# Optimization experiments

Measured on AMD Instinct MI355X. Metric: run time of the kernel, lower is better.

## Reference

```python
import jax, jax.numpy as jnp
import numpy as np

N_NODES = 50000
N_EDGES = 600000
D = 128  # input_nf = output_nf = hidden_nf
EDGE_IN = 2 * D + 1   # source, target, radial
NODE_IN = 2 * D       # x, agg


def _glorot(key, shape):
    fan_in, fan_out = shape[0], shape[1]
    lim = float(np.sqrt(6.0 / (fan_in + fan_out)))
    return jax.random.uniform(key, shape, jnp.float32, -lim, lim)


def setup_inputs() -> dict:
    key = jax.random.key(0)
    ks = jax.random.split(key, 16)
    h = jax.random.normal(ks[0], (N_NODES, D), jnp.float32)
    edge_index = jax.random.randint(ks[1], (2, N_EDGES), 0, N_NODES, jnp.int64 if jax.config.read('jax_enable_x64') else jnp.int32)
    coord = jax.random.uniform(ks[2], (N_NODES, 3), jnp.float32)
    l = jnp.array([10.0, 10.0, 10.0], jnp.float32)  # periodic box lengths (non-trainable buffer)
    return {
        'h': h, 'edge_index': edge_index, 'coord': coord, 'num_nodes': N_NODES, 'l': l,
        # edge_mlp: Linear(257,128) SiLU Linear(128,128) SiLU
        'We1': _glorot(ks[3], (EDGE_IN, D)), 'be1': jnp.zeros((D,), jnp.float32),
        'We2': _glorot(ks[4], (D, D)),       'be2': jnp.zeros((D,), jnp.float32),
        # node_mlp: Linear(256,128) SiLU Linear(128,128)
        'Wn1': _glorot(ks[5], (NODE_IN, D)), 'bn1': jnp.zeros((D,), jnp.float32),
        'Wn2': _glorot(ks[6], (D, D)),       'bn2': jnp.zeros((D,), jnp.float32),
        # coord_mlp: Linear(128,128) SiLU Linear(128,1, bias=False, xavier gain=0.001)
        'Wc1': _glorot(ks[7], (D, D)),       'bc1': jnp.zeros((D,), jnp.float32),
        'Wc2': _glorot(ks[8], (D, 1)) * 0.001,
    }


def reference(h, edge_index, coord, num_nodes, l,
              We1, be1, We2, be2, Wn1, bn1, Wn2, bn2, Wc1, bc1, Wc2):
    row, col = edge_index[0], edge_index[1]

    # coord2radial with periodic minimum-image wrap
    diff = coord[row] - coord[col]                       # [E, 3]
    diff = jnp.where(diff > 0.5 * l, diff - l, diff)
    diff = jnp.where(diff < -0.5 * l, diff + l, diff)
    radial = jnp.sum(diff * diff, axis=1, keepdims=True)  # [E, 1]

    # edge model: gather -> concat -> 2-layer SiLU MLP
    eh = jnp.concatenate([h[row], h[col], radial], axis=1)  # [E, 257]
    eh = jax.nn.silu(eh @ We1 + be1)
    edge_feat = jax.nn.silu(eh @ We2 + be2)                 # [E, 128]

    # coord model: trans/agg computed in the original but discarded (dead code);
    # only the periodic remainder of coord is returned.
    coord_out = jnp.remainder(coord, l)

    # node model: scatter-add edge features into nodes, then MLP + residual
    agg = jax.ops.segment_sum(edge_feat, row, num_segments=num_nodes)  # [N, 128]
    nh = jnp.concatenate([h, agg], axis=1)                              # [N, 256]
    nh = jax.nn.silu(nh @ Wn1 + bn1)
    h_out = h + (nh @ Wn2 + bn2)

    return h_out, coord_out, edge_feat
```

## Files before the change

kernel.cpp:

```cpp
#include <hip/hip_runtime.h>
#include <math.h>

#define D 128
#define SXS 264
#define SHS 132
#define SFS 132

typedef unsigned int u32;
typedef unsigned short u16;
typedef __attribute__((ext_vector_type(8))) short bf16x8;
typedef __attribute__((ext_vector_type(4))) float f32x4;

__device__ __forceinline__ float bfl(u32 u) { return __uint_as_float(u << 16); }
__device__ __forceinline__ float bfh(u32 u) { return __uint_as_float(u & 0xFFFF0000u); }
__device__ __forceinline__ u16 f2bf(float f) {
    u32 u = __float_as_uint(f);
    return (u16)((u + 0x7FFFu + ((u >> 16) & 1u)) >> 16);
}
__device__ __forceinline__ u32 cvt_pk_bf16(float lo, float hi) {
    u32 r;
    asm("v_cvt_pk_bf16_f32 %0, %1, %2" : "=v"(r) : "v"(lo), "v"(hi));
    return r;
}
__device__ __forceinline__ u16 cvt1_bf16(float v) { return (u16)cvt_pk_bf16(v, v); }
__device__ __forceinline__ float silu_f(float x) { return x / (1.0f + __expf(-x)); }

__global__ void coord_kernel(const float* __restrict__ coord,
                             const float* __restrict__ lbox,
                             float* __restrict__ out, int n3) {
    int i = blockIdx.x * 256 + threadIdx.x;
    if (i < n3) {
        float ld = lbox[i % 3];
        float c = coord[i];
        float r = fmodf(c, ld);
        if (r < 0.f) r += ld;
        out[i] = r;
    }
}

__global__ void prep_weights(const float* __restrict__ We1, const float* __restrict__ We2,
                             const float* __restrict__ Wn1, const float* __restrict__ Wn2,
                             u16* __restrict__ wt) {
    int i = blockIdx.x * 256 + threadIdx.x;
    if (i < 32768)        { int n = i >> 8, k = i & 255;              wt[i] = f2bf(We1[(size_t)k*D + n]); }
    else if (i < 49152)   { int j = i - 32768; int n = j >> 7, k = j & 127; wt[i] = f2bf(We2[(size_t)k*D + n]); }
    else if (i < 81920)   { int j = i - 49152; int n = j >> 8, k = j & 255; wt[i] = f2bf(Wn1[(size_t)k*D + n]); }
    else if (i < 98304)   { int j = i - 81920; int n = j >> 7, k = j & 127; wt[i] = f2bf(Wn2[(size_t)k*D + n]); }
}

__global__ void hist_kernel(const int* __restrict__ ei, int* __restrict__ cnt, int E) {
    int e = blockIdx.x * 256 + threadIdx.x;
    if (e < E) atomicAdd(&cnt[ei[e]], 1);
}

__global__ void scan1_kernel(const int* __restrict__ cnt, int* __restrict__ offs,
                             int* __restrict__ bsum, int n ) {
    __shared__ int s[256];
    int t = threadIdx.x, b = blockIdx.x;
    int base = b * 1024 + t * 4;
    int v[4];
    #pragma unroll
    for (int i = 0; i < 4; ++i) { int idx = base + i; v[i] = (idx < n - 1) ? cnt[idx] : 0; }
    int lsum = v[0] + v[1] + v[2] + v[3];
    s[t] = lsum; __syncthreads();
    #pragma unroll
    for (int off = 1; off < 256; off <<= 1) {
        int x = (t >= off) ? s[t - off] : 0; __syncthreads();
        s[t] += x; __syncthreads();
    }
    int run = s[t] - lsum;
    #pragma unroll
    for (int i = 0; i < 4; ++i) { int idx = base + i; if (idx < n) offs[idx] = run; run += v[i]; }
    if (t == 255) bsum[b] = s[255];
}

__global__ void scan2_kernel(int* __restrict__ bsum, int nb) {
    __shared__ int s[64];
    int t = threadIdx.x;
    int orig = (t < nb) ? bsum[t] : 0;
    s[t] = orig; __syncthreads();
    #pragma unroll
    for (int off = 1; off < 64; off <<= 1) {
        int x = (t >= off) ? s[t - off] : 0; __syncthreads();
        s[t] += x; __syncthreads();
    }
    if (t < nb) bsum[t] = s[t] - orig;
}

__global__ void scan3_kernel(int* __restrict__ offs, const int* __restrict__ bsum,
                             int* __restrict__ cursor, int n) {
    int i = blockIdx.x * 256 + threadIdx.x;
    if (i < n) {
        int v = offs[i] + bsum[i >> 10];
        offs[i] = v;
        if (i < n - 1) cursor[i] = v;
    }
}

__global__ void scatter_kernel(const int* __restrict__ ei, int* __restrict__ cursor,
                               int* __restrict__ perm, int E) {
    int e = blockIdx.x * 256 + threadIdx.x;
    if (e < E) { int p = atomicAdd(&cursor[ei[e]], 1); perm[p] = e; }
}

__global__ __launch_bounds__(256, 4) void pq_kernel(
    const float* __restrict__ h, const u16* __restrict__ wt,
    const float* __restrict__ be1,
    u16* __restrict__ Pt, u16* __restrict__ Qt,
    int* __restrict__ cursor, int N)
{
    __shared__ __align__(16) u16 sA[64 * SHS];
    __shared__ __align__(16) u16 sO[64 * SHS];

    const int t = threadIdx.x;
    const int lane = t & 63;
    const int wid = t >> 6;
    const int n0 = blockIdx.x * 64;

    if (t < 64) { int zi = n0 + t; if (zi < N) cursor[zi] = 0; }

    {
        const int e = t & 63, q = t >> 6;
        int ng = n0 + e; int ns = (ng < N) ? ng : N - 1;
        const float4* src = (const float4*)(h + (size_t)ns * D + q * 32);
        u16* dst = sA + e * SHS + q * 32;
        #pragma unroll
        for (int c = 0; c < 4; ++c) {
            float4 a = src[2 * c], b = src[2 * c + 1];
            *(uint4*)(dst + c * 8) = make_uint4(cvt_pk_bf16(a.x, a.y), cvt_pk_bf16(a.z, a.w),
                                               cvt_pk_bf16(b.x, b.y), cvt_pk_bf16(b.z, b.w));
        }
    }
    __syncthreads();

    const int lrow = lane & 15;
    const int kg = lane >> 4;
    const int g4 = kg * 4;
    const int nbase = wid * 32;

    f32x4 accP[4][2] = {}, accQ[4][2] = {};
    {
        bf16x8 Bt[8], Bm[8];
        #pragma unroll
        for (int nn = 0; nn < 2; ++nn)
            #pragma unroll
            for (int s = 0; s < 4; ++s) {
                const u16* bp = wt + (size_t)(nbase + nn * 16 + lrow) * 256 + s * 32 + kg * 8;
                Bt[nn * 4 + s] = *(const bf16x8*)bp;
                Bm[nn * 4 + s] = *(const bf16x8*)(bp + 128);
            }
        #pragma unroll
        for (int s = 0; s < 4; ++s) {
            bf16x8 a[4];
            #pragma unroll
            for (int m = 0; m < 4; ++m)
                a[m] = *(const bf16x8*)(sA + (m * 16 + lrow) * SHS + s * 32 + kg * 8);
            #pragma unroll
            for (int m = 0; m < 4; ++m)
                #pragma unroll
                for (int nn = 0; nn < 2; ++nn) {
                    accP[m][nn] = __builtin_amdgcn_mfma_f32_16x16x32_bf16(a[m], Bt[nn * 4 + s], accP[m][nn], 0, 0, 0);
                    accQ[m][nn] = __builtin_amdgcn_mfma_f32_16x16x32_bf16(a[m], Bm[nn * 4 + s], accQ[m][nn], 0, 0, 0);
                }
        }
    }

    #pragma unroll
    for (int nn = 0; nn < 2; ++nn) {
        int outc = nbase + nn * 16 + lrow;
        float bb = be1[outc];
        #pragma unroll
        for (int m = 0; m < 4; ++m)
            #pragma unroll
            for (int r = 0; r < 4; ++r)
                sO[(m * 16 + g4 + r) * SHS + outc] = cvt1_bf16(accP[m][nn][r] + bb);
    }
    __syncthreads();
    {
        const int f4 = t & 15, rb = t >> 4;
        #pragma unroll
        for (int p = 0; p < 4; ++p) {
            int row = rb + p * 16;
            int ng = n0 + row;
            if (ng < N)
                *(uint4*)(Pt + (size_t)ng * D + f4 * 8) = *(const uint4*)(sO + row * SHS + f4 * 8);
        }
    }
    __syncthreads();
    #pragma unroll
    for (int nn = 0; nn < 2; ++nn) {
        int outc = nbase + nn * 16 + lrow;
        #pragma unroll
        for (int m = 0; m < 4; ++m)
            #pragma unroll
            for (int r = 0; r < 4; ++r)
                sO[(m * 16 + g4 + r) * SHS + outc] = cvt1_bf16(accQ[m][nn][r]);
    }
    __syncthreads();
    {
        const int f4 = t & 15, rb = t >> 4;
        #pragma unroll
        for (int p = 0; p < 4; ++p) {
            int row = rb + p * 16;
            int ng = n0 + row;
            if (ng < N)
                *(uint4*)(Qt + (size_t)ng * D + f4 * 8) = *(const uint4*)(sO + row * SHS + f4 * 8);
        }
    }
}

__global__ __launch_bounds__(256, 8) void edge_pq_kernel(
    const u16* __restrict__ Pt, const u16* __restrict__ Qt,
    const int* __restrict__ ei, const int* __restrict__ perm,
    const float* __restrict__ coord, const float* __restrict__ lbox,
    const u16* __restrict__ wt, const float* __restrict__ We1,
    const float* __restrict__ be2,
    float* __restrict__ ef_out, float* __restrict__ aggf, int E)
{
    __shared__ __align__(16) u16 uni[64 * SHS];
    __shared__ int srow[64], scol[64], sEid[64];
    __shared__ float sRad[64];
    __shared__ float sW[128];
    u16* sH1 = uni;
    u16* sE16 = uni;

    const int t = threadIdx.x;
    const int lane = t & 63;
    const int wid = t >> 6;

    int p0;
    {
        const int nwg = gridDim.x;
        const int orig = blockIdx.x;
        const int q = nwg >> 3, r = nwg & 7;
        const int xcd = orig & 7, idx = orig >> 3;
        const int tile = (xcd < r ? xcd * (q + 1) : r * (q + 1) + (xcd - r) * q) + idx;
        p0 = tile * 64;
    }

    if (t < 64) {
        int slot = p0 + t;
        int eg = perm[(slot < E) ? slot : (E - 1)];
        sEid[t] = (p0 + t < E) ? eg : -1;
        int rr = ei[eg];
        int cc = ei[(size_t)E + eg];
        srow[t] = rr;
        scol[t] = cc;
        float rad = 0.f;
        #pragma unroll
        for (int d3 = 0; d3 < 3; ++d3) {
            float df = coord[(size_t)rr * 3 + d3] - coord[(size_t)cc * 3 + d3];
            float ld = lbox[d3];
            df = (df >  0.5f * ld) ? df - ld : df;
            df = (df < -0.5f * ld) ? df + ld : df;
            rad += df * df;
        }
        sRad[t] = rad;
    } else if (t < 192) {
        sW[t - 64] = We1[(size_t)256 * D + (t - 64)];
    }
    __syncthreads();

    {
        const int e = t & 63, q = t >> 6;
        const u16* Pp = Pt + (size_t)srow[e] * D;
        const u16* Qp = Qt + (size_t)scol[e] * D;
        const float rad = sRad[e];
        #pragma unroll
        for (int c0 = 0; c0 < 4; ++c0) {
            int j0 = q * 32 + c0 * 8;
            uint4 pu = *(const uint4*)(Pp + j0);
            uint4 qu = *(const uint4*)(Qp + j0);
            u32 pa[4] = {pu.x, pu.y, pu.z, pu.w};
            u32 qa[4] = {qu.x, qu.y, qu.z, qu.w};
            u32 ow[4];
            #pragma unroll
            for (int k = 0; k < 4; ++k) {
                float w0 = sW[j0 + 2 * k], w1 = sW[j0 + 2 * k + 1];
                float v0 = silu_f(bfl(pa[k]) + bfl(qa[k]) + rad * w0);
                float v1 = silu_f(bfh(pa[k]) + bfh(qa[k]) + rad * w1);
                ow[k] = cvt_pk_bf16(v0, v1);
            }
            *(uint4*)(sH1 + e * SHS + j0) = make_uint4(ow[0], ow[1], ow[2], ow[3]);
        }
    }
    __syncthreads();

    const int lrow = lane & 15;
    const int kg = lane >> 4;
    const int g4 = kg * 4;
    const int nbase = wid * 32;

    f32x4 acc2[4][2] = {};
    {
        bf16x8 B2[8];
        #pragma unroll
        for (int nn = 0; nn < 2; ++nn)
            #pragma unroll
            for (int s = 0; s < 4; ++s)
                B2[nn * 4 + s] = *(const bf16x8*)(wt + 32768 + (size_t)(nbase + nn * 16 + lrow) * 128 + s * 32 + kg * 8);
        #pragma unroll
        for (int s = 0; s < 4; ++s) {
            bf16x8 a[4];
            #pragma unroll
            for (int m = 0; m < 4; ++m)
                a[m] = *(const bf16x8*)(sH1 + (m * 16 + lrow) * SHS + s * 32 + kg * 8);
            #pragma unroll
            for (int m = 0; m < 4; ++m)
                #pragma unroll
                for (int nn = 0; nn < 2; ++nn)
                    acc2[m][nn] = __builtin_amdgcn_mfma_f32_16x16x32_bf16(a[m], B2[nn * 4 + s], acc2[m][nn], 0, 0, 0);
        }
    }
    __syncthreads();

    #pragma unroll
    for (int nn = 0; nn < 2; ++nn) {
        int outc = nbase + nn * 16 + lrow;
        float bb = be2[outc];
        #pragma unroll
        for (int m = 0; m < 4; ++m)
            #pragma unroll
            for (int r = 0; r < 4; ++r)
                sE16[(m * 16 + g4 + r) * SHS + outc] = cvt1_bf16(silu_f(acc2[m][nn][r] + bb));
    }
    __syncthreads();

    {
        const int ct = t & 127;
        const int half = t >> 7;
        const int ebeg = half * 32, eend = ebeg + 32;
        float run = 0.f;
        int prev = srow[ebeg];
        for (int e = ebeg; e < eend; ++e) {
            int r = srow[e];
            if (r != prev) {
                if (run != 0.f) atomicAdd(&aggf[(size_t)prev * D + ct], run);
                run = 0.f; prev = r;
            }
            int eg = sEid[e];
            if (eg >= 0) {
                float v = __uint_as_float((u32)sE16[e * SHS + ct] << 16);
                __builtin_nontemporal_store(v, &ef_out[(size_t)eg * D + ct]);
                run += v;
            }
        }
        if (run != 0.f) atomicAdd(&aggf[(size_t)prev * D + ct], run);
    }
}

__global__ __launch_bounds__(256, 3) void edge_fb_kernel(
    const float* __restrict__ h,
    const int* __restrict__ ei, const int* __restrict__ perm,
    const float* __restrict__ coord, const float* __restrict__ lbox,
    const u16* __restrict__ wt,
    const float* __restrict__ We1, const float* __restrict__ be1,
    const float* __restrict__ be2,
    float* __restrict__ ef_out, float* __restrict__ aggf, int E)
{
    __shared__ __align__(16) u16 sX[64 * SXS];
    __shared__ __align__(16) u16 sH1[64 * SHS];
    __shared__ int srow[64], scol[64], sEid[64];
    __shared__ float sRad[64];

    const int t = threadIdx.x;
    const int lane = t & 63;
    const int wid = t >> 6;

    int p0;
    {
        const int nwg = gridDim.x;
        const int orig = blockIdx.x;
        const int q = nwg >> 3, r = nwg & 7;
        const int xcd = orig & 7, idx = orig >> 3;
        const int tile = (xcd < r ? xcd * (q + 1) : r * (q + 1) + (xcd - r) * q) + idx;
        p0 = tile * 64;
    }

    if (t < 64) {
        int slot = p0 + t;
        int eg = perm[(slot < E) ? slot : (E - 1)];
        sEid[t] = (p0 + t < E) ? eg : -1;
        srow[t] = ei[eg];
        scol[t] = ei[(size_t)E + eg];
    }
    __syncthreads();

    {
        const int e = t & 63;
        const int q = t >> 6;
        const int r = srow[e], c = scol[e];
        const float4* src = (const float4*)((q < 2) ? (h + (size_t)r * D + (q & 1) * 64)
                                                    : (h + (size_t)c * D + (q & 1) * 64));
        u16* dst = sX + e * SXS + q * 64;
        #pragma unroll
        for (int i = 0; i < 8; ++i) {
            float4 a = src[2 * i], b = src[2 * i + 1];
            *(uint4*)(dst + i * 8) = make_uint4(cvt_pk_bf16(a.x, a.y), cvt_pk_bf16(a.z, a.w),
                                               cvt_pk_bf16(b.x, b.y), cvt_pk_bf16(b.z, b.w));
        }
        if (t < 64) {
            int rr = srow[t], cc = scol[t];
            float rad = 0.f;
            #pragma unroll
            for (int d3 = 0; d3 < 3; ++d3) {
                float df = coord[(size_t)rr * 3 + d3] - coord[(size_t)cc * 3 + d3];
                float ld = lbox[d3];
                df = (df >  0.5f * ld) ? df - ld : df;
                df = (df < -0.5f * ld) ? df + ld : df;
                rad += df * df;
            }
            sRad[t] = rad;
        }
    }
    __syncthreads();

    const int lrow = lane & 15;
    const int kg = lane >> 4;
    const int g4 = kg * 4;
    const int nbase = wid * 32;

    f32x4 acc[4][2] = {};
    {
        bf16x8 B1[16];
        #pragma unroll
        for (int nn = 0; nn < 2; ++nn)
            #pragma unroll
            for (int s = 0; s < 8; ++s)
                B1[nn * 8 + s] = *(const bf16x8*)(wt + (size_t)(nbase + nn * 16 + lrow) * 256 + s * 32 + kg * 8);
        #pragma unroll
        for (int s = 0; s < 8; ++s) {
            bf16x8 a[4];
            #pragma unroll
            for (int m = 0; m < 4; ++m)
                a[m] = *(const bf16x8*)(sX + (m * 16 + lrow) * SXS + s * 32 + kg * 8);
            #pragma unroll
            for (int m = 0; m < 4; ++m)
                #pragma unroll
                for (int nn = 0; nn < 2; ++nn)
                    acc[m][nn] = __builtin_amdgcn_mfma_f32_16x16x32_bf16(a[m], B1[nn * 8 + s], acc[m][nn], 0, 0, 0);
        }
    }

    #pragma unroll
    for (int nn = 0; nn < 2; ++nn) {
        int outc = nbase + nn * 16 + lrow;
        float wl = We1[(size_t)256 * D + outc];
        float bb = be1[outc];
        #pragma unroll
        for (int m = 0; m < 4; ++m)
            #pragma unroll
            for (int r = 0; r < 4; ++r) {
                int e = m * 16 + g4 + r;
                float v = acc[m][nn][r] + sRad[e] * wl + bb;
                sH1[e * SHS + outc] = cvt1_bf16(silu_f(v));
            }
    }
    __syncthreads();

    f32x4 acc2[4][2] = {};
    {
        bf16x8 B2[8];
        #pragma unroll
        for (int nn = 0; nn < 2; ++nn)
            #pragma unroll
            for (int s = 0; s < 4; ++s)
                B2[nn * 4 + s] = *(const bf16x8*)(wt + 32768 + (size_t)(nbase + nn * 16 + lrow) * 128 + s * 32 + kg * 8);
        #pragma unroll
        for (int s = 0; s < 4; ++s) {
            bf16x8 a[4];
            #pragma unroll
            for (int m = 0; m < 4; ++m)
                a[m] = *(const bf16x8*)(sH1 + (m * 16 + lrow) * SHS + s * 32 + kg * 8);
            #pragma unroll
            for (int m = 0; m < 4; ++m)
                #pragma unroll
                for (int nn = 0; nn < 2; ++nn)
                    acc2[m][nn] = __builtin_amdgcn_mfma_f32_16x16x32_bf16(a[m], B2[nn * 4 + s], acc2[m][nn], 0, 0, 0);
        }
    }
    __syncthreads();

    float* sXf = (float*)sX;
    #pragma unroll
    for (int nn = 0; nn < 2; ++nn) {
        int outc = nbase + nn * 16 + lrow;
        float bb = be2[outc];
        #pragma unroll
        for (int m = 0; m < 4; ++m)
            #pragma unroll
            for (int r = 0; r < 4; ++r)
                sXf[(m * 16 + g4 + r) * SFS + outc] = silu_f(acc2[m][nn][r] + bb);
    }
    __syncthreads();

    {
        const int ct = t & 127;
        const int half = t >> 7;
        const int ebeg = half * 32, eend = ebeg + 32;
        float run = 0.f;
        int prev = srow[ebeg];
        for (int e = ebeg; e < eend; ++e) {
            int r = srow[e];
            if (r != prev) {
                if (run != 0.f) atomicAdd(&aggf[(size_t)prev * D + ct], run);
                run = 0.f; prev = r;
            }
            int eg = sEid[e];
            if (eg >= 0) {
                float v = sXf[e * SFS + ct];
                __builtin_nontemporal_store(v, &ef_out[(size_t)eg * D + ct]);
                run += v;
            }
        }
        if (run != 0.f) atomicAdd(&aggf[(size_t)prev * D + ct], run);
    }
}

__global__ __launch_bounds__(256, 4) void node_kernel(
    const float* __restrict__ h, const float* __restrict__ aggf,
    const u16* __restrict__ wt,
    const float* __restrict__ bn1, const float* __restrict__ bn2,
    float* __restrict__ h_out, int N)
{
    __shared__ __align__(16) u16 uni[64 * SXS];
    u16* sX = uni;
    u16* sH1 = uni;
    float* sXf = (float*)uni;

    const int t = threadIdx.x;
    const int lane = t & 63;
    const int wid = t >> 6;
    const int n0 = blockIdx.x * 64;

    {
        const int e = t & 63;
        const int q = t >> 6;
        int ng = n0 + e; int ns = (ng < N) ? ng : N - 1;
        const float4* src = (const float4*)(((q < 2) ? h : aggf) + (size_t)ns * D + (q & 1) * 64);
        u16* dst = sX + e * SXS + q * 64;
        #pragma unroll
        for (int i = 0; i < 8; ++i) {
            float4 a = src[2 * i], b = src[2 * i + 1];
            *(uint4*)(dst + i * 8) = make_uint4(cvt_pk_bf16(a.x, a.y), cvt_pk_bf16(a.z, a.w),
                                               cvt_pk_bf16(b.x, b.y), cvt_pk_bf16(b.z, b.w));
        }
    }
    __syncthreads();

    const int lrow = lane & 15;
    const int kg = lane >> 4;
    const int g4 = kg * 4;
    const int nbase = wid * 32;

    f32x4 acc[4][2] = {};
    {
        bf16x8 B1[16];
        #pragma unroll
        for (int nn = 0; nn < 2; ++nn)
            #pragma unroll
            for (int s = 0; s < 8; ++s)
                B1[nn * 8 + s] = *(const bf16x8*)(wt + 49152 + (size_t)(nbase + nn * 16 + lrow) * 256 + s * 32 + kg * 8);
        #pragma unroll
        for (int s = 0; s < 8; ++s) {
            bf16x8 a[4];
            #pragma unroll
            for (int m = 0; m < 4; ++m)
                a[m] = *(const bf16x8*)(sX + (m * 16 + lrow) * SXS + s * 32 + kg * 8);
            #pragma unroll
            for (int m = 0; m < 4; ++m)
                #pragma unroll
                for (int nn = 0; nn < 2; ++nn)
                    acc[m][nn] = __builtin_amdgcn_mfma_f32_16x16x32_bf16(a[m], B1[nn * 8 + s], acc[m][nn], 0, 0, 0);
        }
    }
    __syncthreads();

    #pragma unroll
    for (int nn = 0; nn < 2; ++nn) {
        int outc = nbase + nn * 16 + lrow;
        float bb = bn1[outc];
        #pragma unroll
        for (int m = 0; m < 4; ++m)
            #pragma unroll
            for (int r = 0; r < 4; ++r)
                sH1[(m * 16 + g4 + r) * SHS + outc] = cvt1_bf16(silu_f(acc[m][nn][r] + bb));
    }
    __syncthreads();

    f32x4 acc2[4][2] = {};
    {
        bf16x8 B2[8];
        #pragma unroll
        for (int nn = 0; nn < 2; ++nn)
            #pragma unroll
            for (int s = 0; s < 4; ++s)
                B2[nn * 4 + s] = *(const bf16x8*)(wt + 81920 + (size_t)(nbase + nn * 16 + lrow) * 128 + s * 32 + kg * 8);
        #pragma unroll
        for (int s = 0; s < 4; ++s) {
            bf16x8 a[4];
            #pragma unroll
            for (int m = 0; m < 4; ++m)
                a[m] = *(const bf16x8*)(sH1 + (m * 16 + lrow) * SHS + s * 32 + kg * 8);
            #pragma unroll
            for (int m = 0; m < 4; ++m)
                #pragma unroll
                for (int nn = 0; nn < 2; ++nn)
                    acc2[m][nn] = __builtin_amdgcn_mfma_f32_16x16x32_bf16(a[m], B2[nn * 4 + s], acc2[m][nn], 0, 0, 0);
        }
    }
    __syncthreads();

    #pragma unroll
    for (int nn = 0; nn < 2; ++nn) {
        int outc = nbase + nn * 16 + lrow;
        float bb = bn2[outc];
        #pragma unroll
        for (int m = 0; m < 4; ++m)
            #pragma unroll
            for (int r = 0; r < 4; ++r)
                sXf[(m * 16 + g4 + r) * SFS + outc] = acc2[m][nn][r] + bb;
    }
    __syncthreads();

    {
        const int f4 = t & 31;
        const int nb = t >> 5;
        #pragma unroll
        for (int i = 0; i < 8; ++i) {
            int nl = nb + i * 8;
            int ng = n0 + nl;
            if (ng < N) {
                f32x4 v = *(const f32x4*)&sXf[nl * SFS + f4 * 4];
                const f32x4 hv = *(const f32x4*)&h[(size_t)ng * D + f4 * 4];
                v += hv;
                __builtin_nontemporal_store(v, (f32x4*)&h_out[(size_t)ng * D + f4 * 4]);
            }
        }
    }
}

extern "C" void kernel_launch(void* const* d_in, const int* in_sizes, int n_in,
                              void* d_out, int out_size, void* d_ws, size_t ws_size,
                              hipStream_t stream) {
    const float* h     = (const float*)d_in[0];
    const int*   ei    = (const int*)d_in[1];
    const float* coord = (const float*)d_in[2];
    const float* lbox  = (const float*)d_in[4];
    const float* We1   = (const float*)d_in[5];
    const float* be1   = (const float*)d_in[6];
    const float* We2   = (const float*)d_in[7];
    const float* be2   = (const float*)d_in[8];
    const float* Wn1   = (const float*)d_in[9];
    const float* bn1   = (const float*)d_in[10];
    const float* Wn2   = (const float*)d_in[11];
    const float* bn2   = (const float*)d_in[12];

    const int N = in_sizes[0] / D;
    const int E = in_sizes[1] / 2;

    float* out       = (float*)d_out;
    float* h_out     = out;
    float* coord_out = out + (size_t)N * D;
    float* ef_out    = coord_out + (size_t)N * 3;
    float* aggf      = h_out;

    int* wsi = (int*)d_ws;
    u16* wt     = (u16*)d_ws;
    int* offs   = wsi + 49152;
    int* cursor = offs + (N + 8);
    int* bsum   = cursor + (N + 8);
    int* perm   = bsum + 64;
    u16* Pt     = (u16*)(perm + E);
    u16* Qt     = Pt + (size_t)N * D;

    size_t need = (size_t)((char*)(Qt + (size_t)N * D) - (char*)d_ws);
    const bool use_pq = ws_size >= need;

    const int nb1 = (N + 1 + 1023) / 1024;

    prep_weights<<<384, 256, 0, stream>>>(We1, We2, Wn1, Wn2, wt);
    if (use_pq)
        pq_kernel<<<(N + 63) / 64, 256, 0, stream>>>(h, wt, be1, Pt, Qt, cursor, N);
    else
        hipMemsetAsync(cursor, 0, (size_t)N * sizeof(int), stream);
    coord_kernel<<<(N * 3 + 255) / 256, 256, 0, stream>>>(coord, lbox, coord_out, N * 3);

    hipMemsetAsync(aggf, 0, (size_t)N * D * sizeof(float), stream);

    hist_kernel<<<(E + 255) / 256, 256, 0, stream>>>(ei, cursor, E);
    scan1_kernel<<<nb1, 256, 0, stream>>>(cursor, offs, bsum, N + 1);
    scan2_kernel<<<1, 64, 0, stream>>>(bsum, nb1);
    scan3_kernel<<<(N + 1 + 255) / 256, 256, 0, stream>>>(offs, bsum, cursor, N + 1);
    scatter_kernel<<<(E + 255) / 256, 256, 0, stream>>>(ei, cursor, perm, E);

    if (use_pq)
        edge_pq_kernel<<<(E + 63) / 64, 256, 0, stream>>>(
            Pt, Qt, ei, perm, coord, lbox, wt, We1, be2, ef_out, aggf, E);
    else
        edge_fb_kernel<<<(E + 63) / 64, 256, 0, stream>>>(
            h, ei, perm, coord, lbox, wt, We1, be1, be2, ef_out, aggf, E);

    node_kernel<<<(N + 63) / 64, 256, 0, stream>>>(
        h, aggf, wt, bn1, bn2, h_out, N);
}
```

Measured before the change: 274.7 us.

## Fuse setup launches into one kernel and shrink node kernel shared memory

Merges the weight conversion, coord remainder, aggregate zeroing and cursor zeroing into a single setup kernel, replacing separate launches and memsets. The node kernel now runs its first GEMM in two K-halves (h, then agg) through a half-size shared buffer and raises its occupancy target to 6 blocks per CU. Its second-layer output is staged as bf16 instead of fp32, which adds rounding error to h_out. Edge-kernel index loads are marked nontemporal.

```diff
diff --git a/kernel.cpp b/kernel.cpp
--- a/kernel.cpp
+++ b/kernel.cpp
@@ -25,27 +25,39 @@
 __device__ __forceinline__ u16 cvt1_bf16(float v) { return (u16)cvt_pk_bf16(v, v); }
 __device__ __forceinline__ float silu_f(float x) { return x / (1.0f + __expf(-x)); }
 
-__global__ void coord_kernel(const float* __restrict__ coord,
-                             const float* __restrict__ lbox,
-                             float* __restrict__ out, int n3) {
-    int i = blockIdx.x * 256 + threadIdx.x;
-    if (i < n3) {
-        float ld = lbox[i % 3];
-        float c = coord[i];
-        float r = fmodf(c, ld);
-        if (r < 0.f) r += ld;
-        out[i] = r;
-    }
-}
-
-__global__ void prep_weights(const float* __restrict__ We1, const float* __restrict__ We2,
-                             const float* __restrict__ Wn1, const float* __restrict__ Wn2,
-                             u16* __restrict__ wt) {
-    int i = blockIdx.x * 256 + threadIdx.x;
-    if (i < 32768)        { int n = i >> 8, k = i & 255;              wt[i] = f2bf(We1[(size_t)k*D + n]); }
-    else if (i < 49152)   { int j = i - 32768; int n = j >> 7, k = j & 127; wt[i] = f2bf(We2[(size_t)k*D + n]); }
-    else if (i < 81920)   { int j = i - 49152; int n = j >> 8, k = j & 255; wt[i] = f2bf(Wn1[(size_t)k*D + n]); }
-    else if (i < 98304)   { int j = i - 81920; int n = j >> 7, k = j & 127; wt[i] = f2bf(Wn2[(size_t)k*D + n]); }
+__global__ __launch_bounds__(256) void setup_kernel(
+    const float* __restrict__ We1, const float* __restrict__ We2,
+    const float* __restrict__ Wn1, const float* __restrict__ Wn2,
+    u16* __restrict__ wt,
+    const float* __restrict__ coord, const float* __restrict__ lbox,
+    float* __restrict__ coord_out, int n3,
+    float* __restrict__ aggf, int nAgg4,
+    int* __restrict__ cursor, int N,
+    int B1, int B2, int B3)
+{
+    const int b = blockIdx.x, t = threadIdx.x;
+    if (b < B1) {
+        int i = b * 256 + t;
+        if (i < 32768)        { int n = i >> 8, k = i & 255;              wt[i] = f2bf(We1[(size_t)k*D + n]); }
+        else if (i < 49152)   { int j = i - 32768; int n = j >> 7, k = j & 127; wt[i] = f2bf(We2[(size_t)k*D + n]); }
+        else if (i < 81920)   { int j = i - 49152; int n = j >> 8, k = j & 255; wt[i] = f2bf(Wn1[(size_t)k*D + n]); }
+        else                  { int j = i - 81920; int n = j >> 7, k = j & 127; wt[i] = f2bf(Wn2[(size_t)k*D + n]); }
+    } else if (b < B2) {
+        int i = (b - B1) * 256 + t;
+        if (i < n3) {
+            float ld = lbox[i % 3];
+            float c = coord[i];
+            float r = fmodf(c, ld);
+            if (r < 0.f) r += ld;
+            coord_out[i] = r;
+        }
+    } else if (b < B3) {
+        int i = (b - B2) * 256 + t;
+        if (i < nAgg4) ((f32x4*)aggf)[i] = (f32x4){0.f, 0.f, 0.f, 0.f};
+    } else {
+        int i = (b - B3) * 256 + t;
+        if (i < N) cursor[i] = 0;
+    }
 }
 
 __global__ void hist_kernel(const int* __restrict__ ei, int* __restrict__ cnt, int E) {
@@ -106,8 +118,7 @@
 __global__ __launch_bounds__(256, 4) void pq_kernel(
     const float* __restrict__ h, const u16* __restrict__ wt,
     const float* __restrict__ be1,
-    u16* __restrict__ Pt, u16* __restrict__ Qt,
-    int* __restrict__ cursor, int N)
+    u16* __restrict__ Pt, u16* __restrict__ Qt, int N)
 {
     __shared__ __align__(16) u16 sA[64 * SHS];
     __shared__ __align__(16) u16 sO[64 * SHS];
@@ -116,8 +127,6 @@
     const int lane = t & 63;
     const int wid = t >> 6;
     const int n0 = blockIdx.x * 64;
-
-    if (t < 64) { int zi = n0 + t; if (zi < N) cursor[zi] = 0; }
 
     {
         const int e = t & 63, q = t >> 6;
@@ -240,10 +249,10 @@
 
     if (t < 64) {
         int slot = p0 + t;
-        int eg = perm[(slot < E) ? slot : (E - 1)];
+        int eg = __builtin_nontemporal_load(&perm[(slot < E) ? slot : (E - 1)]);
         sEid[t] = (p0 + t < E) ? eg : -1;
-        int rr = ei[eg];
-        int cc = ei[(size_t)E + eg];
+        int rr = __builtin_nontemporal_load(&ei[eg]);
+        int cc = __builtin_nontemporal_load(&ei[(size_t)E + eg]);
         srow[t] = rr;
         scol[t] = cc;
         float rad = 0.f;
@@ -517,61 +526,93 @@
     }
 }
 
-__global__ __launch_bounds__(256, 4) void node_kernel(
+__global__ __launch_bounds__(256, 6) void node_kernel(
     const float* __restrict__ h, const float* __restrict__ aggf,
     const u16* __restrict__ wt,
     const float* __restrict__ bn1, const float* __restrict__ bn2,
     float* __restrict__ h_out, int N)
 {
-    __shared__ __align__(16) u16 uni[64 * SXS];
-    u16* sX = uni;
-    u16* sH1 = uni;
-    float* sXf = (float*)uni;
+    __shared__ __align__(16) u16 uni[64 * SHS];
 
     const int t = threadIdx.x;
     const int lane = t & 63;
     const int wid = t >> 6;
     const int n0 = blockIdx.x * 64;
 
-    {
-        const int e = t & 63;
-        const int q = t >> 6;
-        int ng = n0 + e; int ns = (ng < N) ? ng : N - 1;
-        const float4* src = (const float4*)(((q < 2) ? h : aggf) + (size_t)ns * D + (q & 1) * 64);
-        u16* dst = sX + e * SXS + q * 64;
-        #pragma unroll
-        for (int i = 0; i < 8; ++i) {
-            float4 a = src[2 * i], b = src[2 * i + 1];
-            *(uint4*)(dst + i * 8) = make_uint4(cvt_pk_bf16(a.x, a.y), cvt_pk_bf16(a.z, a.w),
-                                               cvt_pk_bf16(b.x, b.y), cvt_pk_bf16(b.z, b.w));
-        }
-    }
-    __syncthreads();
-
     const int lrow = lane & 15;
     const int kg = lane >> 4;
     const int g4 = kg * 4;
     const int nbase = wid * 32;
 
+    const int se = t & 63, sq = t >> 6;
+    const int sng = n0 + se;
+    const int sns = (sng < N) ? sng : N - 1;
+
+    {
+        const float4* src = (const float4*)(h + (size_t)sns * D + sq * 32);
+        u16* dst = uni + se * SHS + sq * 32;
+        #pragma unroll
+        for (int c = 0; c < 4; ++c) {
+            float4 a = src[2 * c], b = src[2 * c + 1];
+            *(uint4*)(dst + c * 8) = make_uint4(cvt_pk_bf16(a.x, a.y), cvt_pk_bf16(a.z, a.w),
+                                               cvt_pk_bf16(b.x, b.y), cvt_pk_bf16(b.z, b.w));
+        }
+    }
+    __syncthreads();
+
     f32x4 acc[4][2] = {};
     {
-        bf16x8 B1[16];
+        bf16x8 B1[8];
         #pragma unroll
         for (int nn = 0; nn < 2; ++nn)
             #pragma unroll
-            for (int s = 0; s < 8; ++s)
-                B1[nn * 8 + s] = *(const bf16x8*)(wt + 49152 + (size_t)(nbase + nn * 16 + lrow) * 256 + s * 32 + kg * 8);
-        #pragma unroll
-        for (int s = 0; s < 8; ++s) {
+            for (int s = 0; s < 4; ++s)
+                B1[nn * 4 + s] = *(const bf16x8*)(wt + 49152 + (size_t)(nbase + nn * 16 + lrow) * 256 + s * 32 + kg * 8);
+        #pragma unroll
+        for (int s = 0; s < 4; ++s) {
             bf16x8 a[4];
             #pragma unroll
             for (int m = 0; m < 4; ++m)
-                a[m] = *(const bf16x8*)(sX + (m * 16 + lrow) * SXS + s * 32 + kg * 8);
+                a[m] = *(const bf16x8*)(uni + (m * 16 + lrow) * SHS + s * 32 + kg * 8);
             #pragma unroll
             for (int m = 0; m < 4; ++m)
                 #pragma unroll
                 for (int nn = 0; nn < 2; ++nn)
-                    acc[m][nn] = __builtin_amdgcn_mfma_f32_16x16x32_bf16(a[m], B1[nn * 8 + s], acc[m][nn], 0, 0, 0);
+                    acc[m][nn] = __builtin_amdgcn_mfma_f32_16x16x32_bf16(a[m], B1[nn * 4 + s], acc[m][nn], 0, 0, 0);
+        }
+    }
+    __syncthreads();
+
+    {
+        const float4* src = (const float4*)(aggf + (size_t)sns * D + sq * 32);
+        u16* dst = uni + se * SHS + sq * 32;
+        #pragma unroll
+        for (int c = 0; c < 4; ++c) {
+            float4 a = src[2 * c], b = src[2 * c + 1];
+            *(uint4*)(dst + c * 8) = make_uint4(cvt_pk_bf16(a.x, a.y), cvt_pk_bf16(a.z, a.w),
+                                               cvt_pk_bf16(b.x, b.y), cvt_pk_bf16(b.z, b.w));
+        }
+    }
+    __syncthreads();
+
+    {
+        bf16x8 B1[8];
+        #pragma unroll
+        for (int nn = 0; nn < 2; ++nn)
+            #pragma unroll
+            for (int s = 0; s < 4; ++s)
+                B1[nn * 4 + s] = *(const bf16x8*)(wt + 49152 + (size_t)(nbase + nn * 16 + lrow) * 256 + 128 + s * 32 + kg * 8);
+        #pragma unroll
+        for (int s = 0; s < 4; ++s) {
+            bf16x8 a[4];
+            #pragma unroll
+            for (int m = 0; m < 4; ++m)
+                a[m] = *(const bf16x8*)(uni + (m * 16 + lrow) * SHS + s * 32 + kg * 8);
+            #pragma unroll
+            for (int m = 0; m < 4; ++m)
+                #pragma unroll
+                for (int nn = 0; nn < 2; ++nn)
+                    acc[m][nn] = __builtin_amdgcn_mfma_f32_16x16x32_bf16(a[m], B1[nn * 4 + s], acc[m][nn], 0, 0, 0);
         }
     }
     __syncthreads();
@@ -584,7 +625,7 @@
         for (int m = 0; m < 4; ++m)
             #pragma unroll
             for (int r = 0; r < 4; ++r)
-                sH1[(m * 16 + g4 + r) * SHS + outc] = cvt1_bf16(silu_f(acc[m][nn][r] + bb));
+                uni[(m * 16 + g4 + r) * SHS + outc] = cvt1_bf16(silu_f(acc[m][nn][r] + bb));
     }
     __syncthreads();
 
@@ -601,7 +642,7 @@
             bf16x8 a[4];
             #pragma unroll
             for (int m = 0; m < 4; ++m)
-                a[m] = *(const bf16x8*)(sH1 + (m * 16 + lrow) * SHS + s * 32 + kg * 8);
+                a[m] = *(const bf16x8*)(uni + (m * 16 + lrow) * SHS + s * 32 + kg * 8);
             #pragma unroll
             for (int m = 0; m < 4; ++m)
                 #pragma unroll
@@ -619,7 +660,7 @@
         for (int m = 0; m < 4; ++m)
             #pragma unroll
             for (int r = 0; r < 4; ++r)
-                sXf[(m * 16 + g4 + r) * SFS + outc] = acc2[m][nn][r] + bb;
+                uni[(m * 16 + g4 + r) * SHS + outc] = cvt1_bf16(acc2[m][nn][r] + bb);
     }
     __syncthreads();
 
@@ -631,9 +672,13 @@
             int nl = nb + i * 8;
             int ng = n0 + nl;
             if (ng < N) {
-                f32x4 v = *(const f32x4*)&sXf[nl * SFS + f4 * 4];
+                const ushort4 mv = *(const ushort4*)(uni + nl * SHS + f4 * 4);
                 const f32x4 hv = *(const f32x4*)&h[(size_t)ng * D + f4 * 4];
-                v += hv;
+                f32x4 v;
+                v[0] = hv[0] + __uint_as_float((u32)mv.x << 16);
+                v[1] = hv[1] + __uint_as_float((u32)mv.y << 16);
+                v[2] = hv[2] + __uint_as_float((u32)mv.z << 16);
+                v[3] = hv[3] + __uint_as_float((u32)mv.w << 16);
                 __builtin_nontemporal_store(v, (f32x4*)&h_out[(size_t)ng * D + f4 * 4]);
             }
         }
@@ -679,14 +724,18 @@
 
     const int nb1 = (N + 1 + 1023) / 1024;
 
-    prep_weights<<<384, 256, 0, stream>>>(We1, We2, Wn1, Wn2, wt);
+    const int n3 = N * 3;
+    const int nAgg4 = N * D / 4;
+    const int B1 = 384;
+    const int B2 = B1 + (n3 + 255) / 256;
+    const int B3 = B2 + (nAgg4 + 255) / 256;
+    const int Bt = B3 + (N + 255) / 256;
+    setup_kernel<<<Bt, 256, 0, stream>>>(We1, We2, Wn1, Wn2, wt,
+                                         coord, lbox, coord_out, n3,
+                                         aggf, nAgg4, cursor, N, B1, B2, B3);
+
     if (use_pq)
-        pq_kernel<<<(N + 63) / 64, 256, 0, stream>>>(h, wt, be1, Pt, Qt, cursor, N);
-    else
-        hipMemsetAsync(cursor, 0, (size_t)N * sizeof(int), stream);
-    coord_kernel<<<(N * 3 + 255) / 256, 256, 0, stream>>>(coord, lbox, coord_out, N * 3);
-
-    hipMemsetAsync(aggf, 0, (size_t)N * D * sizeof(float), stream);
+        pq_kernel<<<(N + 63) / 64, 256, 0, stream>>>(h, wt, be1, Pt, Qt, N);
 
     hist_kernel<<<(E + 255) / 256, 256, 0, stream>>>(ei, cursor, E);
     scan1_kernel<<<nb1, 256, 0, stream>>>(cursor, offs, bsum, N + 1);
```

Result: slower. 296.7 us (+8.0%).
